# Kernel optimization log

Hardware: AMD Instinct MI355X
Metric: run time of the kernel (lower is better)

The kernel has to match this reference:

```python
import jax, jax.numpy as jnp
import numpy as np

TAU_S = 3.0
DT_MAX = 5.0
BATCH, N, D = 64, 16384, 256


def setup_inputs() -> dict:
    key = jax.random.key(0)
    k1, k2, k3 = jax.random.split(key, 3)
    # query spike times in [0, 20) ms, matching the pattern_times range (5, 20)
    query_times = jax.random.uniform(k1, (BATCH, D), dtype=jnp.float32) * 20.0
    patterns = jax.random.normal(k2, (N, D), dtype=jnp.float32) * 0.1
    weights = jnp.ones((D,), dtype=jnp.float32)
    return {"query_times": query_times, "patterns": patterns, "weights": weights}


def reference(query_times, patterns, weights):
    # pattern spike times in (5, 20) ms
    pattern_times = 20.0 - 15.0 * jax.nn.sigmoid(patterns)  # (N, d)
    # broadcast difference: (batch, N, d)
    dt = query_times[:, None, :] - pattern_times[None, :, :]
    adt = jnp.abs(dt)
    # temporal kernel: exp decay inside coincidence window, zero outside
    kappa = jnp.where(adt < DT_MAX, jnp.exp(-adt / TAU_S), 0.0)
    w = jnp.abs(weights)  # (d,)
    # weighted reduce over d -> (batch, N)
    S = jnp.einsum("bnd,d->bn", kappa, w)
    return S
```

## Files before the change

kernel.cpp:

```cpp
#include <hip/hip_runtime.h>
#include <hip/hip_bf16.h>


static constexpr float kC2    = 0.48089834696298783f;
static constexpr float kL2E   = 1.4426950408889634f;
static constexpr float kTheta = 0.18887560283756183f;

#define B_   64
#define N_   16384
#define D_   256
#define NCH  64

__global__ __launch_bounds__(256) void pre_pattern(const float* __restrict__ patterns,
                                                   _Float16* __restrict__ pat2) {
    const int n = blockIdx.x;
    const int d = threadIdx.x;
    float x  = patterns[(size_t)n * D_ + d];
    float t  = exp2f(-x * kL2E);
    float sg = __fdividef(1.0f, 1.0f + t);
    float u  = fmaf(-15.0f * kC2, sg, 20.0f * kC2);
    float e0 = exp2f(u);
    float i0 = exp2f(-u);
    int dc = d >> 2, j = d & 3;
    size_t base = ((size_t)dc * N_ + n) * 8;
    pat2[base + j]     = (_Float16)e0;
    pat2[base + 4 + j] = (_Float16)i0;
}

__global__ __launch_bounds__(256) void pre_query(const float* __restrict__ q,
                                                 float* __restrict__ qarr) {
    const int b = blockIdx.x;
    const int d = threadIdx.x;
    float qv = q[(size_t)b * D_ + d];
    float u  = qv * kC2;
    int dc = d >> 2, j = d & 3, bg = b >> 2, b4 = b & 3;
    size_t idx = ((size_t)(dc * 16 + bg) << 5) + b4 * 8 + j * 2;
    qarr[idx]     = exp2f(u);
    qarr[idx + 1] = exp2f(-u);
}

struct QBuf { float q[32]; float w[4]; };

__device__ __forceinline__ void load_q(const float* __restrict__ qarr,
                                       const float* __restrict__ weights,
                                       int dc, int bg, QBuf& o) {
    const float* p = qarr + ((size_t)(dc * 16 + bg) << 5);
#pragma unroll
    for (int j = 0; j < 32; ++j) o.q[j] = p[j];
#pragma unroll
    for (int j = 0; j < 4; ++j) o.w[j] = fabsf(weights[dc * 4 + j]);
}

__device__ __forceinline__ void chunk_math(const QBuf& Q, uint4 r0, uint4 r1,
                                           float acc[2][4]) {
    union Cv { uint4 u; _Float16 h[8]; };
    Cv c0, c1; c0.u = r0; c1.u = r1;
    float ep[2][4], ip[2][4];
#pragma unroll
    for (int j = 0; j < 4; ++j) {
        ep[0][j] = (float)c0.h[j];  ip[0][j] = (float)c0.h[j + 4];
        ep[1][j] = (float)c1.h[j];  ip[1][j] = (float)c1.h[j + 4];
    }
#pragma unroll
    for (int b = 0; b < 4; ++b) {
#pragma unroll
        for (int j = 0; j < 4; ++j) {
            float Eq = Q.q[b * 8 + j * 2];
            float Iq = Q.q[b * 8 + j * 2 + 1];
#pragma unroll
            for (int r = 0; r < 2; ++r) {
                float a = Eq * ip[r][j];
                float c = Iq * ep[r][j];
                float k = fminf(a, c);
                float m = (k > kTheta) ? k : 0.0f;
                acc[r][b] = fmaf(m, Q.w[j], acc[r][b]);
            }
        }
    }
}

__global__ __launch_bounds__(256, 2) void cd_main(
        const uint4* __restrict__ pat2,
        const float* __restrict__ qarr,
        const float* __restrict__ weights,
        float* __restrict__ S) {
    const int l    = threadIdx.x & 63;
    const int wv   = threadIdx.x >> 6;
    const int nt   = blockIdx.x >> 2;
    const int bsub = blockIdx.x & 3;
    const int bg   = __builtin_amdgcn_readfirstlane(bsub * 4 + wv);
    const int b0   = bg * 4;
    const int n0   = nt * 128;
    const int row0 = n0 + l, row1 = n0 + 64 + l;

    float acc[2][4];
#pragma unroll
    for (int r = 0; r < 2; ++r)
#pragma unroll
        for (int b = 0; b < 4; ++b) acc[r][b] = 0.0f;

    QBuf qA, qB;
    uint4 pA0, pA1, pB0, pB1;
    load_q(qarr, weights, 0, bg, qA);
    pA0 = pat2[(size_t)0 * N_ + row0];
    pA1 = pat2[(size_t)0 * N_ + row1];

    for (int dc = 0; dc < NCH - 2; dc += 2) {
        load_q(qarr, weights, dc + 1, bg, qB);
        pB0 = pat2[(size_t)(dc + 1) * N_ + row0];
        pB1 = pat2[(size_t)(dc + 1) * N_ + row1];
        chunk_math(qA, pA0, pA1, acc);
        load_q(qarr, weights, dc + 2, bg, qA);
        pA0 = pat2[(size_t)(dc + 2) * N_ + row0];
        pA1 = pat2[(size_t)(dc + 2) * N_ + row1];
        chunk_math(qB, pB0, pB1, acc);
    }
    load_q(qarr, weights, NCH - 1, bg, qB);
    pB0 = pat2[(size_t)(NCH - 1) * N_ + row0];
    pB1 = pat2[(size_t)(NCH - 1) * N_ + row1];
    chunk_math(qA, pA0, pA1, acc);
    chunk_math(qB, pB0, pB1, acc);

#pragma unroll
    for (int r = 0; r < 2; ++r)
#pragma unroll
        for (int b = 0; b < 4; ++b)
            S[(size_t)(b0 + b) * N_ + n0 + r * 64 + l] = acc[r][b];
}

extern "C" void kernel_launch(void* const* d_in, const int* in_sizes, int n_in,
                              void* d_out, int out_size, void* d_ws, size_t ws_size,
                              hipStream_t stream) {
    const float* q        = (const float*)d_in[0];
    const float* patterns = (const float*)d_in[1];
    const float* weights  = (const float*)d_in[2];
    float* S = (float*)d_out;

    float*    qarr = (float*)d_ws;
    _Float16* pat2 = (_Float16*)((char*)d_ws + (size_t)NCH * 16 * 32 * 4);

    pre_pattern<<<N_, 256, 0, stream>>>(patterns, pat2);
    pre_query  <<<B_, 256, 0, stream>>>(q, qarr);
    cd_main    <<<512, 256, 0, stream>>>((const uint4*)pat2, qarr, weights, S);
}
```

Baseline: 135.3 us.

## Tile pattern layout per 64-row block and halve rows per thread in main kernel

After: 128.3 us. -5.2%, faster.

```diff
diff --git a/kernel.cpp b/kernel.cpp
--- a/kernel.cpp
+++ b/kernel.cpp
@@ -10,21 +10,30 @@
 #define N_   16384
 #define D_   256
 #define NCH  64
+#define NTL  256
 
 __global__ __launch_bounds__(256) void pre_pattern(const float* __restrict__ patterns,
-                                                   _Float16* __restrict__ pat2) {
-    const int n = blockIdx.x;
-    const int d = threadIdx.x;
-    float x  = patterns[(size_t)n * D_ + d];
-    float t  = exp2f(-x * kL2E);
-    float sg = __fdividef(1.0f, 1.0f + t);
-    float u  = fmaf(-15.0f * kC2, sg, 20.0f * kC2);
-    float e0 = exp2f(u);
-    float i0 = exp2f(-u);
-    int dc = d >> 2, j = d & 3;
-    size_t base = ((size_t)dc * N_ + n) * 8;
-    pat2[base + j]     = (_Float16)e0;
-    pat2[base + 4 + j] = (_Float16)i0;
+                                                   uint4* __restrict__ pat2) {
+    const int nt  = blockIdx.x;
+    const int tid = threadIdx.x;
+#pragma unroll
+    for (int it = 0; it < 16; ++it) {
+        int idx = it * 256 + tid;
+        int dc  = idx >> 6;
+        int row = idx & 63;
+        float4 x4 = *(const float4*)&patterns[((size_t)nt * 64 + row) * D_ + dc * 4];
+        float xs[4] = {x4.x, x4.y, x4.z, x4.w};
+        union { uint4 u; _Float16 h[8]; } o;
+#pragma unroll
+        for (int j = 0; j < 4; ++j) {
+            float t  = exp2f(-xs[j] * kL2E);
+            float sg = __fdividef(1.0f, 1.0f + t);
+            float u  = fmaf(-15.0f * kC2, sg, 20.0f * kC2);
+            o.h[j]     = (_Float16)exp2f(u);
+            o.h[4 + j] = (_Float16)exp2f(-u);
+        }
+        pat2[(size_t)nt * 4096 + dc * 64 + row] = o.u;
+    }
 }
 
 __global__ __launch_bounds__(256) void pre_query(const float* __restrict__ q,
@@ -51,81 +60,64 @@
     for (int j = 0; j < 4; ++j) o.w[j] = fabsf(weights[dc * 4 + j]);
 }
 
-__device__ __forceinline__ void chunk_math(const QBuf& Q, uint4 r0, uint4 r1,
-                                           float acc[2][4]) {
-    union Cv { uint4 u; _Float16 h[8]; };
-    Cv c0, c1; c0.u = r0; c1.u = r1;
-    float ep[2][4], ip[2][4];
+__device__ __forceinline__ void chunk_math(const QBuf& Q, uint4 r0, float acc[4]) {
+    union { uint4 u; _Float16 h[8]; } c; c.u = r0;
+    float ep[4], ip[4];
 #pragma unroll
     for (int j = 0; j < 4; ++j) {
-        ep[0][j] = (float)c0.h[j];  ip[0][j] = (float)c0.h[j + 4];
-        ep[1][j] = (float)c1.h[j];  ip[1][j] = (float)c1.h[j + 4];
+        ep[j] = (float)c.h[j];
+        ip[j] = (float)c.h[j + 4];
     }
 #pragma unroll
     for (int b = 0; b < 4; ++b) {
 #pragma unroll
         for (int j = 0; j < 4; ++j) {
-            float Eq = Q.q[b * 8 + j * 2];
-            float Iq = Q.q[b * 8 + j * 2 + 1];
-#pragma unroll
-            for (int r = 0; r < 2; ++r) {
-                float a = Eq * ip[r][j];
-                float c = Iq * ep[r][j];
-                float k = fminf(a, c);
-                float m = (k > kTheta) ? k : 0.0f;
-                acc[r][b] = fmaf(m, Q.w[j], acc[r][b]);
-            }
+            float a = Q.q[b * 8 + j * 2]     * ip[j];
+            float c2 = Q.q[b * 8 + j * 2 + 1] * ep[j];
+            float k = fminf(a, c2);
+            float m = (k > kTheta) ? k : 0.0f;
+            acc[b] = fmaf(m, Q.w[j], acc[b]);
         }
     }
 }
 
-__global__ __launch_bounds__(256, 2) void cd_main(
+__global__ __launch_bounds__(256, 4) void cd_main(
         const uint4* __restrict__ pat2,
         const float* __restrict__ qarr,
         const float* __restrict__ weights,
         float* __restrict__ S) {
     const int l    = threadIdx.x & 63;
     const int wv   = threadIdx.x >> 6;
-    const int nt   = blockIdx.x >> 2;
-    const int bsub = blockIdx.x & 3;
+    const int nt   = blockIdx.x & 255;
+    const int bsub = blockIdx.x >> 8;
     const int bg   = __builtin_amdgcn_readfirstlane(bsub * 4 + wv);
     const int b0   = bg * 4;
-    const int n0   = nt * 128;
-    const int row0 = n0 + l, row1 = n0 + 64 + l;
 
-    float acc[2][4];
-#pragma unroll
-    for (int r = 0; r < 2; ++r)
-#pragma unroll
-        for (int b = 0; b < 4; ++b) acc[r][b] = 0.0f;
+    const uint4* pbase = pat2 + (size_t)nt * 4096 + l;
+
+    float acc[4] = {0.f, 0.f, 0.f, 0.f};
 
     QBuf qA, qB;
-    uint4 pA0, pA1, pB0, pB1;
+    uint4 pA, pB;
     load_q(qarr, weights, 0, bg, qA);
-    pA0 = pat2[(size_t)0 * N_ + row0];
-    pA1 = pat2[(size_t)0 * N_ + row1];
+    pA = pbase[0];
 
     for (int dc = 0; dc < NCH - 2; dc += 2) {
         load_q(qarr, weights, dc + 1, bg, qB);
-        pB0 = pat2[(size_t)(dc + 1) * N_ + row0];
-        pB1 = pat2[(size_t)(dc + 1) * N_ + row1];
-        chunk_math(qA, pA0, pA1, acc);
+        pB = pbase[(dc + 1) * 64];
+        chunk_math(qA, pA, acc);
         load_q(qarr, weights, dc + 2, bg, qA);
-        pA0 = pat2[(size_t)(dc + 2) * N_ + row0];
-        pA1 = pat2[(size_t)(dc + 2) * N_ + row1];
-        chunk_math(qB, pB0, pB1, acc);
+        pA = pbase[(dc + 2) * 64];
+        chunk_math(qB, pB, acc);
     }
     load_q(qarr, weights, NCH - 1, bg, qB);
-    pB0 = pat2[(size_t)(NCH - 1) * N_ + row0];
-    pB1 = pat2[(size_t)(NCH - 1) * N_ + row1];
-    chunk_math(qA, pA0, pA1, acc);
-    chunk_math(qB, pB0, pB1, acc);
+    pB = pbase[(NCH - 1) * 64];
+    chunk_math(qA, pA, acc);
+    chunk_math(qB, pB, acc);
 
 #pragma unroll
-    for (int r = 0; r < 2; ++r)
-#pragma unroll
-        for (int b = 0; b < 4; ++b)
-            S[(size_t)(b0 + b) * N_ + n0 + r * 64 + l] = acc[r][b];
+    for (int b = 0; b < 4; ++b)
+        S[(size_t)(b0 + b) * N_ + nt * 64 + l] = acc[b];
 }
 
 extern "C" void kernel_launch(void* const* d_in, const int* in_sizes, int n_in,
@@ -136,10 +128,10 @@
     const float* weights  = (const float*)d_in[2];
     float* S = (float*)d_out;
 
-    float*    qarr = (float*)d_ws;
-    _Float16* pat2 = (_Float16*)((char*)d_ws + (size_t)NCH * 16 * 32 * 4);
+    float* qarr = (float*)d_ws;
+    uint4* pat2 = (uint4*)((char*)d_ws + (size_t)NCH * 16 * 32 * 4);
 
-    pre_pattern<<<N_, 256, 0, stream>>>(patterns, pat2);
-    pre_query  <<<B_, 256, 0, stream>>>(q, qarr);
-    cd_main    <<<512, 256, 0, stream>>>((const uint4*)pat2, qarr, weights, S);
+    pre_pattern<<<NTL, 256, 0, stream>>>(patterns, pat2);
+    pre_query  <<<B_,  256, 0, stream>>>(q, qarr);
+    cd_main    <<<1024, 256, 0, stream>>>(pat2, qarr, weights, S);
 }
```
